# Optimization experiments

Hardware: AMD Instinct MI355X
Metric: run time of the kernel (lower is better)

## Reference

```python
import jax, jax.numpy as jnp
import numpy as np

B, N, D, H, DH, E, BIAS_DIM = 8, 512, 512, 8, 64, 32768, 8

def setup_inputs() -> dict:
    key = jax.random.key(0)
    ks = jax.random.split(key, 10)
    states = jax.random.normal(ks[0], (B, N, D), jnp.float32)
    key_states = jax.random.normal(ks[1], (B, N, D), jnp.float32)
    # causal mask, broadcastable over heads: [B,1,N,N]
    masks = jnp.broadcast_to(jnp.tril(jnp.ones((N, N), jnp.float32)), (B, 1, N, N))
    edge_type = jax.random.randint(ks[2], (E, 1), 0, BIAS_DIM, jnp.int32)
    b_idx = jax.random.randint(ks[3], (E, 1), 0, B, jnp.int32)
    q_idx = jax.random.randint(ks[4], (E, 1), 0, N, jnp.int32)
    k_idx = jax.random.randint(ks[5], (E, 1), 0, N, jnp.int32)
    attention_bias = jnp.concatenate([edge_type, b_idx, q_idx, k_idx], axis=1)
    s = 0.05
    Wq = jax.random.normal(ks[6], (D, H, DH), jnp.float32) * s
    Wk = jax.random.normal(ks[7], (D, H, DH), jnp.float32) * s
    Wv = jax.random.normal(ks[8], (D, H, DH), jnp.float32) * s
    k2 = jax.random.split(ks[9], 3)
    Wo = jax.random.normal(k2[0], (H, DH, D), jnp.float32) * s
    bias_embs = jax.random.normal(k2[1], (BIAS_DIM, DH), jnp.float32) * s
    bias_scalar = jax.random.normal(k2[2], (DH, 1), jnp.float32) * s
    return {"states": states, "key_states": key_states, "masks": masks,
            "attention_bias": attention_bias, "Wq": Wq, "Wk": Wk, "Wv": Wv,
            "Wo": Wo, "bias_embs": bias_embs, "bias_scalar": bias_scalar}

def reference(states, key_states, masks, attention_bias, Wq, Wk, Wv, Wo, bias_embs, bias_scalar):
    q = jnp.einsum('btd,dha->btha', states, Wq)
    k = jnp.einsum('btd,dha->btha', key_states, Wk)
    v = jnp.einsum('btd,dha->btha', key_states, Wv)
    alpha = jnp.einsum('bkha,bqha->bhqk', k, q)  # [B,H,Q,K]
    # sparse edge bias: embed edge types, project to scalar, scatter into [B,Q,K]
    et = attention_bias[:, 0]
    bias_vals = (bias_embs[et] @ bias_scalar)[:, 0]  # [E]
    bq, bk = alpha.shape[2], alpha.shape[3]
    bias_mat = jnp.zeros((alpha.shape[0], bq, bk), alpha.dtype)
    bias_mat = bias_mat.at[attention_bias[:, 1], attention_bias[:, 2], attention_bias[:, 3]].add(bias_vals)
    summed_keys = jnp.sum(k, axis=-1)  # [B,K,H]
    alpha = alpha + jnp.einsum('bqk,bkh->bhqk', bias_mat, summed_keys)
    alpha = alpha * jax.lax.rsqrt(jnp.float32(DH))
    neg = jnp.finfo(jnp.float32).min
    alpha = alpha * masks + (1.0 - jnp.ceil(masks)) * neg
    alpha = jax.nn.softmax(alpha, axis=-1)
    alpha = alpha * masks
    context = jnp.einsum('bhqk,bkha->bqha', alpha, v)
    return jnp.einsum('btha,had->btd', context, Wo)
```

## Files before the change

### kernel.cpp

```cpp
#include <hip/hip_runtime.h>

typedef unsigned short u16;
typedef unsigned int u32;
typedef __bf16 bf16x8 __attribute__((ext_vector_type(8)));
typedef float f32x4 __attribute__((ext_vector_type(4)));
typedef u16 u16x8 __attribute__((ext_vector_type(8)));
typedef u16 u16x4 __attribute__((ext_vector_type(4)));


__device__ __forceinline__ u16 f2b(float f) {
  union { float f; u32 i; } v; v.f = f;
  u32 r = v.i + 0x7fffu + ((v.i >> 16) & 1u);
  return (u16)(r >> 16);
}
__device__ __forceinline__ float b2f(u16 u) {
  union { u32 i; float f; } v; v.i = ((u32)u) << 16; return v.f;
}

#define GLL16(gp, lp)                                                      \
  __builtin_amdgcn_global_load_lds(                                       \
      (const __attribute__((address_space(1))) u32*)(gp),                 \
      (__attribute__((address_space(3))) u32*)(lp), 16, 0, 0)

__device__ __forceinline__ void stage64(const u16* g, u16* l, int wave, int lane) {
  int rsub = lane >> 3;
  int gs = (((lane & 7) ^ rsub) << 3);
  #pragma unroll
  for (int c = 0; c < 2; c++) {
    int ch = wave * 2 + c;
    GLL16(g + (size_t)(ch * 8 + rsub) * 512 + gs, l + ch * 512);
  }
}
__device__ __forceinline__ void stage128(const u16* g, u16* l, int wave, int lane) {
  int rsub = lane >> 3;
  int gs = (((lane & 7) ^ rsub) << 3);
  #pragma unroll
  for (int c = 0; c < 4; c++) {
    int ch = wave * 4 + c;
    GLL16(g + (size_t)(ch * 8 + rsub) * 512 + gs, l + ch * 512);
  }
}
__device__ __forceinline__ int swz(int row, int g) {
  return row * 64 + ((g ^ (row & 7)) << 3);
}

__global__ __launch_bounds__(256) void prologue(
    const float* __restrict__ states, const float* __restrict__ key_states,
    const float* __restrict__ Wq, const float* __restrict__ Wk,
    const float* __restrict__ Wv, const float* __restrict__ Wo,
    const int* __restrict__ ab, const float* __restrict__ be,
    const float* __restrict__ bsc,
    u16* __restrict__ sb, u16* __restrict__ kbin, u16* __restrict__ wbase,
    float* __restrict__ bias_mat, int n_edges) {
  __shared__ u16 t[32][33];
  __shared__ float tv[8];
  int bid = blockIdx.x;
  int tid = threadIdx.x;
  if (bid < 2048) {
    const float* src = (bid >= 1024) ? key_states : states;
    u16* dst = (bid >= 1024) ? kbin : sb;
    int gid = (bid & 1023) * 256 + tid;
    const float4* sp = (const float4*)src + (size_t)gid * 2;
    float4 x0 = sp[0], x1 = sp[1];
    u16x8 p;
    p[0] = f2b(x0.x); p[1] = f2b(x0.y); p[2] = f2b(x0.z); p[3] = f2b(x0.w);
    p[4] = f2b(x1.x); p[5] = f2b(x1.y); p[6] = f2b(x1.z); p[7] = f2b(x1.w);
    *(u16x8*)(dst + (size_t)gid * 8) = p;
  } else if (bid < 3072) {
    int tt = bid - 2048;
    int z = tt >> 8, rem = tt & 255;
    int bx = rem & 15, by = rem >> 4;
    const float* src; float sc = 1.f;
    if (z == 0)      { src = Wq; sc = 0.125f; }
    else if (z == 1) { src = Wk; }
    else if (z == 2) { src = Wv; }
    else             { src = Wo; }
    u16* dst = wbase + (size_t)z * 262144;
    int tx = tid & 31, ty = tid >> 5;
    int c0 = bx * 32, r0 = by * 32;
    #pragma unroll
    for (int i = ty; i < 32; i += 8) t[i][tx] = f2b(src[(r0 + i) * 512 + c0 + tx] * sc);
    __syncthreads();
    #pragma unroll
    for (int i = ty; i < 32; i += 8) dst[(c0 + i) * 512 + r0 + tx] = t[tx][i];
  } else {
    if (tid < 8) {
      float s = 0.f;
      #pragma unroll
      for (int a = 0; a < 64; a++) s += be[tid * 64 + a] * bsc[a];
      tv[tid] = s * 0.125f;
    }
    __syncthreads();
    int e = (bid - 3072) * 256 + tid;
    if (e < n_edges) {
      int et = ab[e * 4 + 0];
      int b  = ab[e * 4 + 1];
      int qi = ab[e * 4 + 2];
      int ki = ab[e * 4 + 3];
      atomicAdd(&bias_mat[((size_t)b * 512 + qi) * 512 + ki], tv[et]);
    }
  }
}

__global__ __launch_bounds__(256) void qkv_gemm(const u16* __restrict__ sb,
                                                const u16* __restrict__ kbin,
                                                const u16* __restrict__ wT,
                                                u16* __restrict__ qb,
                                                u16* __restrict__ kbo,
                                                u16* __restrict__ vtb,
                                                float* __restrict__ summed) {
  __shared__ alignas(16) u16 As[2][64 * 64];
  __shared__ alignas(16) u16 Bs[2][128 * 64];
  __shared__ float ssum[4][64];
  int tid = threadIdx.x;
  int lane = tid & 63, wave = tid >> 6;
  int quad = lane >> 4, ln = lane & 15;
  int row0 = blockIdx.x * 64;
  int col0 = blockIdx.y * 128;
  const u16* A = (col0 < 512) ? sb : kbin;
  const u16* Ab = A + (size_t)row0 * 512;
  const u16* Bb = wT + (size_t)col0 * 512;

  f32x4 acc[4][2];
  #pragma unroll
  for (int i = 0; i < 4; i++)
    #pragma unroll
    for (int j = 0; j < 2; j++) acc[i][j] = (f32x4){0.f, 0.f, 0.f, 0.f};

  stage64(Ab, As[0], wave, lane);
  stage128(Bb, Bs[0], wave, lane);

  int cur = 0;
  for (int k0 = 0; k0 < 512; k0 += 64) {
    __syncthreads();
    if (k0 < 448) {
      stage64(Ab + k0 + 64, As[cur ^ 1], wave, lane);
      stage128(Bb + k0 + 64, Bs[cur ^ 1], wave, lane);
    }
    #pragma unroll
    for (int s = 0; s < 2; s++) {
      bf16x8 af[4], bfv[2];
      #pragma unroll
      for (int i = 0; i < 4; i++)
        af[i] = *(bf16x8*)&As[cur][swz(i * 16 + ln, s * 4 + quad)];
      #pragma unroll
      for (int j = 0; j < 2; j++)
        bfv[j] = *(bf16x8*)&Bs[cur][swz(wave * 32 + j * 16 + ln, s * 4 + quad)];
      #pragma unroll
      for (int i = 0; i < 4; i++)
        #pragma unroll
        for (int j = 0; j < 2; j++)
          acc[i][j] = __builtin_amdgcn_mfma_f32_16x16x32_bf16(af[i], bfv[j], acc[i][j], 0, 0, 0);
    }
    cur ^= 1;
  }

  int region = col0 >> 9;
  int nbase = col0 & 511;
  if (region <= 1) {
    u16* Cout = region ? kbo : qb;
    #pragma unroll
    for (int i = 0; i < 4; i++)
      #pragma unroll
      for (int j = 0; j < 2; j++) {
        int mb = row0 + i * 16 + quad * 4;
        int n = nbase + wave * 32 + j * 16 + ln;
        #pragma unroll
        for (int r = 0; r < 4; r++)
          Cout[(size_t)(mb + r) * 512 + n] = f2b(acc[i][j][r]);
      }
    if (region == 1) {
      #pragma unroll
      for (int i = 0; i < 4; i++)
        #pragma unroll
        for (int r = 0; r < 4; r++) {
          float v = acc[i][0][r] + acc[i][1][r];
          v += __shfl_xor(v, 1);
          v += __shfl_xor(v, 2);
          v += __shfl_xor(v, 4);
          v += __shfl_xor(v, 8);
          if (ln == 0) ssum[wave][i * 16 + quad * 4 + r] = v;
        }
      __syncthreads();
      if (tid < 128) {
        int hl = tid >> 6, row = tid & 63;
        float s = ssum[hl * 2][row] + ssum[hl * 2 + 1][row];
        int m = row0 + row;
        int b = m >> 9, t = m & 511;
        int h = (nbase >> 6) + hl;
        summed[((size_t)(b * 8 + h)) * 512 + t] = s;
      }
    }
  } else {
    #pragma unroll
    for (int i = 0; i < 4; i++)
      #pragma unroll
      for (int j = 0; j < 2; j++) {
        int mb = row0 + i * 16 + quad * 4;
        int bb = mb >> 9, t0 = mb & 511;
        int a_abs = nbase + wave * 32 + j * 16 + ln;
        int h = a_abs >> 6, a = a_abs & 63;
        u16x4 p;
        p[0] = f2b(acc[i][j][0]); p[1] = f2b(acc[i][j][1]);
        p[2] = f2b(acc[i][j][2]); p[3] = f2b(acc[i][j][3]);
        *(u16x4*)&vtb[(((size_t)bb * 8 + h) * 64 + a) * 512 + t0] = p;
      }
  }
}

__global__ __launch_bounds__(256) void out_gemm(const u16* __restrict__ A,
                                                const u16* __restrict__ BT,
                                                float* __restrict__ C) {
  __shared__ alignas(16) u16 As[2][64 * 64];
  __shared__ alignas(16) u16 Bs[2][64 * 64];
  int tid = threadIdx.x;
  int lane = tid & 63, wave = tid >> 6;
  int quad = lane >> 4, ln = lane & 15;
  int wr = wave >> 1, wc = wave & 1;
  int row0 = blockIdx.x * 64;
  int col0 = blockIdx.y * 64;
  const u16* Ab = A + (size_t)row0 * 512;
  const u16* Bb = BT + (size_t)col0 * 512;

  f32x4 acc[2][2];
  #pragma unroll
  for (int i = 0; i < 2; i++)
    #pragma unroll
    for (int j = 0; j < 2; j++) acc[i][j] = (f32x4){0.f, 0.f, 0.f, 0.f};

  stage64(Ab, As[0], wave, lane);
  stage64(Bb, Bs[0], wave, lane);

  int cur = 0;
  for (int k0 = 0; k0 < 512; k0 += 64) {
    __syncthreads();
    if (k0 < 448) {
      stage64(Ab + k0 + 64, As[cur ^ 1], wave, lane);
      stage64(Bb + k0 + 64, Bs[cur ^ 1], wave, lane);
    }
    #pragma unroll
    for (int s = 0; s < 2; s++) {
      bf16x8 af[2], bfv[2];
      #pragma unroll
      for (int i = 0; i < 2; i++)
        af[i] = *(bf16x8*)&As[cur][swz(wr * 32 + i * 16 + ln, s * 4 + quad)];
      #pragma unroll
      for (int j = 0; j < 2; j++)
        bfv[j] = *(bf16x8*)&Bs[cur][swz(wc * 32 + j * 16 + ln, s * 4 + quad)];
      #pragma unroll
      for (int i = 0; i < 2; i++)
        #pragma unroll
        for (int j = 0; j < 2; j++)
          acc[i][j] = __builtin_amdgcn_mfma_f32_16x16x32_bf16(af[i], bfv[j], acc[i][j], 0, 0, 0);
    }
    cur ^= 1;
  }
  #pragma unroll
  for (int i = 0; i < 2; i++)
    #pragma unroll
    for (int j = 0; j < 2; j++) {
      int mb = row0 + wr * 32 + i * 16 + quad * 4;
      int n = col0 + wc * 32 + j * 16 + ln;
      #pragma unroll
      for (int r = 0; r < 4; r++)
        C[(size_t)(mb + r) * 512 + n] = acc[i][j][r];
    }
}

__global__ __launch_bounds__(256) void attn_mfma(const u16* __restrict__ q,
                                                 const u16* __restrict__ k,
                                                 const u16* __restrict__ vt,
                                                 const float* __restrict__ bias_mat,
                                                 const float* __restrict__ summed,
                                                 u16* __restrict__ ctx,
                                                 float* __restrict__ Opart,
                                                 float* __restrict__ ml) {
  __shared__ alignas(16) u16 Qs[64 * 64];
  __shared__ alignas(16) u16 Ks[2][64 * 64];
  __shared__ alignas(16) u16 Vs[2][64 * 64];
  __shared__ alignas(16) u16 Ps[4][16 * 72];
  int tid = threadIdx.x;
  int wave = tid >> 6, lane = tid & 63;
  int quad = lane >> 4, ln = lane & 15;
  int p2 = blockIdx.x;
  int bh, u;
  {
    const int fours[6] = {3, 4, 6, 8, 10, 11};
    const int threes[2] = {2, 9};
    const int ones[2] = {0, 5};
    const int twos[2] = {1, 7};
    if (p2 < 384)      { bh = p2 & 63; u = fours[p2 >> 6]; }
    else if (p2 < 512) { int q2 = p2 - 384; bh = q2 & 63; u = threes[q2 >> 6]; }
    else if (p2 < 640) { int q2 = p2 - 512; bh = q2 & 63; u = ones[q2 >> 6]; }
    else               { int q2 = p2 - 640; bh = q2 & 63; u = twos[q2 >> 6]; }
  }
  int b = bh >> 3, h = bh & 7;
  int qt, kb0, kbe, part = 0;
  bool partial;
  if (u < 4) { qt = u; kb0 = 0; kbe = u; partial = false; }
  else {
    int v = u - 4; qt = 4 + (v >> 1); part = v & 1; partial = true;
    if (part == 0) { kb0 = 0; kbe = 3; } else { kb0 = 4; kbe = qt; }
  }
  int q0 = qt * 64;

  const u16* qb_ = q + ((size_t)(b * 512 + q0)) * 512 + h * 64;
  const u16* kb_ = k + ((size_t)(b * 512)) * 512 + h * 64;
  const u16* vb_ = vt + ((size_t)bh * 64) * 512;

  stage64(qb_, Qs, wave, lane);
  stage64(kb_ + (size_t)kb0 * 64 * 512, Ks[0], wave, lane);
  stage64(vb_ + kb0 * 64, Vs[0], wave, lane);

  float m_r[4], l_r[4];
  f32x4 o[4];
  #pragma unroll
  for (int r = 0; r < 4; r++) { m_r[r] = -3.40282347e38f; l_r[r] = 0.f; }
  #pragma unroll
  for (int nt = 0; nt < 4; nt++) o[nt] = (f32x4){0.f, 0.f, 0.f, 0.f};

  int qrow = q0 + wave * 16 + quad * 4;

  float c_skv[4], c_bias[4][4];
  #pragma unroll
  for (int nt = 0; nt < 4; nt++) {
    int t = kb0 * 64 + nt * 16 + ln;
    c_skv[nt] = summed[bh * 512 + t];
    const float* bp2 = bias_mat + ((size_t)(b * 512 + qrow)) * 512 + t;
    #pragma unroll
    for (int r = 0; r < 4; r++) c_bias[nt][r] = bp2[(size_t)r * 512];
  }

  int cur = 0;
  for (int kb = kb0; kb <= kbe; kb++) {
    __syncthreads();

    float n_skv[4], n_bias[4][4];
    if (kb < kbe) {
      stage64(kb_ + (size_t)(kb + 1) * 64 * 512, Ks[cur ^ 1], wave, lane);
      stage64(vb_ + (kb + 1) * 64, Vs[cur ^ 1], wave, lane);
      #pragma unroll
      for (int nt = 0; nt < 4; nt++) {
        int t = (kb + 1) * 64 + nt * 16 + ln;
        n_skv[nt] = summed[bh * 512 + t];
        const float* bp2 = bias_mat + ((size_t)(b * 512 + qrow)) * 512 + t;
        #pragma unroll
        for (int r = 0; r < 4; r++) n_bias[nt][r] = bp2[(size_t)r * 512];
      }
    }

    bf16x8 aq0 = *(bf16x8*)&Qs[swz(wave * 16 + ln, quad)];
    bf16x8 aq1 = *(bf16x8*)&Qs[swz(wave * 16 + ln, 4 + quad)];
    f32x4 s[4];
    #pragma unroll
    for (int nt = 0; nt < 4; nt++) {
      bf16x8 b0 = *(bf16x8*)&Ks[cur][swz(nt * 16 + ln, quad)];
      bf16x8 b1 = *(bf16x8*)&Ks[cur][swz(nt * 16 + ln, 4 + quad)];
      s[nt] = (f32x4){0.f, 0.f, 0.f, 0.f};
      s[nt] = __builtin_amdgcn_mfma_f32_16x16x32_bf16(aq0, b0, s[nt], 0, 0, 0);
      s[nt] = __builtin_amdgcn_mfma_f32_16x16x32_bf16(aq1, b1, s[nt], 0, 0, 0);
    }

    #pragma unroll
    for (int nt = 0; nt < 4; nt++) {
      int t = kb * 64 + nt * 16 + ln;
      #pragma unroll
      for (int r = 0; r < 4; r++) {
        float val = s[nt][r] + c_bias[nt][r] * c_skv[nt];
        s[nt][r] = (t <= qrow + r) ? val : -3.40282347e38f;
      }
    }

    float alpha[4];
    #pragma unroll
    for (int r = 0; r < 4; r++) {
      float tm = fmaxf(fmaxf(s[0][r], s[1][r]), fmaxf(s[2][r], s[3][r]));
      #pragma unroll
      for (int off = 8; off; off >>= 1) tm = fmaxf(tm, __shfl_xor(tm, off));
      float mn = fmaxf(m_r[r], tm);
      alpha[r] = __expf(m_r[r] - mn);
      m_r[r] = mn;
      float rs = 0.f;
      #pragma unroll
      for (int nt = 0; nt < 4; nt++) {
        float pp = __expf(s[nt][r] - mn);
        s[nt][r] = pp;
        rs += pp;
      }
      #pragma unroll
      for (int off = 8; off; off >>= 1) rs += __shfl_xor(rs, off);
      l_r[r] = l_r[r] * alpha[r] + rs;
    }

    #pragma unroll
    for (int nt = 0; nt < 4; nt++)
      #pragma unroll
      for (int r = 0; r < 4; r++)
        Ps[wave][(quad * 4 + r) * 72 + nt * 16 + ln] = f2b(s[nt][r]);
    #pragma unroll
    for (int nt = 0; nt < 4; nt++)
      #pragma unroll
      for (int r = 0; r < 4; r++)
        o[nt][r] *= alpha[r];

    bf16x8 ap0 = *(bf16x8*)&Ps[wave][ln * 72 + quad * 8];
    bf16x8 ap1 = *(bf16x8*)&Ps[wave][ln * 72 + 32 + quad * 8];
    #pragma unroll
    for (int nt = 0; nt < 4; nt++) {
      bf16x8 b0 = *(bf16x8*)&Vs[cur][swz(nt * 16 + ln, quad)];
      bf16x8 b1 = *(bf16x8*)&Vs[cur][swz(nt * 16 + ln, 4 + quad)];
      o[nt] = __builtin_amdgcn_mfma_f32_16x16x32_bf16(ap0, b0, o[nt], 0, 0, 0);
      o[nt] = __builtin_amdgcn_mfma_f32_16x16x32_bf16(ap1, b1, o[nt], 0, 0, 0);
    }

    if (kb < kbe) {
      #pragma unroll
      for (int nt = 0; nt < 4; nt++) {
        c_skv[nt] = n_skv[nt];
        #pragma unroll
        for (int r = 0; r < 4; r++) c_bias[nt][r] = n_bias[nt][r];
      }
    }
    cur ^= 1;
  }

  if (!partial) {
    #pragma unroll
    for (int r = 0; r < 4; r++) {
      float inv = 1.f / l_r[r];
      int qr2 = qrow + r;
      u16* dst = ctx + ((size_t)(b * 512 + qr2)) * 512 + h * 64;
      #pragma unroll
      for (int nt = 0; nt < 4; nt++)
        dst[nt * 16 + ln] = f2b(o[nt][r] * inv);
    }
  } else {
    #pragma unroll
    for (int r = 0; r < 4; r++) {
      int row = qrow + r - 256;
      float* dst = Opart + (((size_t)(part * 64 + bh)) * 256 + row) * 64;
      #pragma unroll
      for (int nt = 0; nt < 4; nt++)
        dst[nt * 16 + ln] = o[nt][r];
    }
    if (ln == 0) {
      #pragma unroll
      for (int r = 0; r < 4; r++) {
        int row = qrow + r - 256;
        float* mp = ml + (((size_t)(part * 64 + bh)) * 256 + row) * 2;
        mp[0] = m_r[r];
        mp[1] = l_r[r];
      }
    }
  }
}

__global__ __launch_bounds__(256) void attn_merge(const float* __restrict__ Opart,
                                                  const float* __restrict__ ml,
                                                  u16* __restrict__ ctx) {
  int gid = blockIdx.x * 256 + threadIdx.x;
  int col = gid & 63;
  int row = (gid >> 6) & 255;
  int bh = gid >> 14;
  size_t i0 = (size_t)bh * 256 + row;
  size_t i1 = (size_t)(64 + bh) * 256 + row;
  float m0 = ml[i0 * 2], l0 = ml[i0 * 2 + 1];
  float m1 = ml[i1 * 2], l1 = ml[i1 * 2 + 1];
  float m = fmaxf(m0, m1);
  float a0 = __expf(m0 - m), a1 = __expf(m1 - m);
  float l = l0 * a0 + l1 * a1;
  float O0 = Opart[i0 * 64 + col], O1 = Opart[i1 * 64 + col];
  float val = (O0 * a0 + O1 * a1) / l;
  int b = bh >> 3, h = bh & 7, qrow = 256 + row;
  ctx[((size_t)(b * 512 + qrow)) * 512 + h * 64 + col] = f2b(val);
}

extern "C" void kernel_launch(void* const* d_in, const int* in_sizes, int n_in,
                              void* d_out, int out_size, void* d_ws, size_t ws_size,
                              hipStream_t stream) {
  const float* states     = (const float*)d_in[0];
  const float* key_states = (const float*)d_in[1];
  const int*   ab         = (const int*)d_in[3];
  const float* Wq         = (const float*)d_in[4];
  const float* Wk         = (const float*)d_in[5];
  const float* Wv         = (const float*)d_in[6];
  const float* Wo         = (const float*)d_in[7];
  const float* be         = (const float*)d_in[8];
  const float* bsc        = (const float*)d_in[9];
  float* out = (float*)d_out;

  char* ws = (char*)d_ws;
  const size_t MB = 1024 * 1024;
  u16* wbase    = (u16*)(ws);
  u16* wot      = (u16*)(ws + 1536 * 1024);
  u16* sb       = (u16*)(ws + 2 * MB);
  u16* kbin     = (u16*)(ws + 6 * MB);
  u16* qb       = (u16*)(ws + 10 * MB);
  u16* kbo      = (u16*)(ws + 14 * MB);
  u16* vtb      = (u16*)(ws + 18 * MB);
  u16* ctxb     = (u16*)(ws + 22 * MB);
  float* bias_m = (float*)(ws + 26 * MB);
  float* summed = (float*)(ws + 34 * MB);
  float* Opart  = (float*)(ws + 35 * MB);
  float* mlbuf  = (float*)(ws + 43 * MB);

  int n_edges = in_sizes[3] / 4;

  hipMemsetAsync(bias_m, 0, (size_t)8 * MB, stream);
  prologue<<<dim3(3072 + (n_edges + 255) / 256), 256, 0, stream>>>(
      states, key_states, Wq, Wk, Wv, Wo, ab, be, bsc, sb, kbin, wbase, bias_m, n_edges);
  qkv_gemm<<<dim3(64, 12), 256, 0, stream>>>(sb, kbin, wbase, qb, kbo, vtb, summed);
  attn_mfma<<<dim3(768), 256, 0, stream>>>(qb, kbo, vtb, bias_m, summed, ctxb, Opart, mlbuf);
  attn_merge<<<dim3(4096), 256, 0, stream>>>(Opart, mlbuf, ctxb);
  out_gemm<<<dim3(64, 8), 256, 0, stream>>>(ctxb, wot, out);
}
```

Before: 134.6 us.

## Fuse bias zeroing, edge scatter and split-softmax merge into neighbouring kernels

Removes the hipMemset and has prologue zero the bias matrix with float4 stores. Moves the edge bias scatter (atomicAdd) into qkv_gemm blocks. Drops the separate attn_merge kernel and merges the split-KV partials inside out_gemm's A-tile staging for rows 256-511. Together these cut two launches and a round trip of ctx through global memory. In exchange, merged tiles use register loads plus LDS stores instead of async global_load_lds, and the atomic scatter delays the start of the GEMM.

```diff
diff --git a/kernel.cpp b/kernel.cpp
--- a/kernel.cpp
+++ b/kernel.cpp
@@ -13,9 +13,6 @@
   u32 r = v.i + 0x7fffu + ((v.i >> 16) & 1u);
   return (u16)(r >> 16);
 }
-__device__ __forceinline__ float b2f(u16 u) {
-  union { u32 i; float f; } v; v.i = ((u32)u) << 16; return v.f;
-}
 
 #define GLL16(gp, lp)                                                      \
   __builtin_amdgcn_global_load_lds(                                       \
@@ -48,12 +45,9 @@
     const float* __restrict__ states, const float* __restrict__ key_states,
     const float* __restrict__ Wq, const float* __restrict__ Wk,
     const float* __restrict__ Wv, const float* __restrict__ Wo,
-    const int* __restrict__ ab, const float* __restrict__ be,
-    const float* __restrict__ bsc,
     u16* __restrict__ sb, u16* __restrict__ kbin, u16* __restrict__ wbase,
-    float* __restrict__ bias_mat, int n_edges) {
+    float* __restrict__ bias_mat) {
   __shared__ u16 t[32][33];
-  __shared__ float tv[8];
   int bid = blockIdx.x;
   int tid = threadIdx.x;
   if (bid < 2048) {
@@ -84,37 +78,53 @@
     #pragma unroll
     for (int i = ty; i < 32; i += 8) dst[(c0 + i) * 512 + r0 + tx] = t[tx][i];
   } else {
-    if (tid < 8) {
-      float s = 0.f;
-      #pragma unroll
-      for (int a = 0; a < 64; a++) s += be[tid * 64 + a] * bsc[a];
-      tv[tid] = s * 0.125f;
-    }
-    __syncthreads();
-    int e = (bid - 3072) * 256 + tid;
-    if (e < n_edges) {
-      int et = ab[e * 4 + 0];
-      int b  = ab[e * 4 + 1];
-      int qi = ab[e * 4 + 2];
-      int ki = ab[e * 4 + 3];
-      atomicAdd(&bias_mat[((size_t)b * 512 + qi) * 512 + ki], tv[et]);
-    }
+    int i = (bid - 3072) * 256 + tid;
+    float4 z4 = {0.f, 0.f, 0.f, 0.f};
+    ((float4*)bias_mat)[i] = z4;
   }
 }
 
 __global__ __launch_bounds__(256) void qkv_gemm(const u16* __restrict__ sb,
                                                 const u16* __restrict__ kbin,
                                                 const u16* __restrict__ wT,
+                                                const int* __restrict__ ab,
+                                                const float* __restrict__ be,
+                                                const float* __restrict__ bsc,
+                                                float* __restrict__ bias_m,
                                                 u16* __restrict__ qb,
                                                 u16* __restrict__ kbo,
                                                 u16* __restrict__ vtb,
-                                                float* __restrict__ summed) {
+                                                float* __restrict__ summed,
+                                                int n_edges) {
   __shared__ alignas(16) u16 As[2][64 * 64];
   __shared__ alignas(16) u16 Bs[2][128 * 64];
   __shared__ float ssum[4][64];
+  __shared__ float tvs[8];
   int tid = threadIdx.x;
   int lane = tid & 63, wave = tid >> 6;
   int quad = lane >> 4, ln = lane & 15;
+  int fb = blockIdx.y * 64 + blockIdx.x;
+
+  if (tid < 8) {
+    const float4* bev = (const float4*)(be + tid * 64);
+    const float4* bscv = (const float4*)bsc;
+    float s = 0.f;
+    #pragma unroll
+    for (int a4 = 0; a4 < 16; a4++) {
+      float4 x = bev[a4], y = bscv[a4];
+      s += x.x * y.x + x.y * y.y + x.z * y.z + x.w * y.w;
+    }
+    tvs[tid] = s * 0.125f;
+  }
+  __syncthreads();
+  for (int e = fb * 256 + tid; e < n_edges; e += 768 * 256) {
+    int et = ab[e * 4 + 0];
+    int b  = ab[e * 4 + 1];
+    int qi = ab[e * 4 + 2];
+    int ki = ab[e * 4 + 3];
+    atomicAdd(&bias_m[((size_t)b * 512 + qi) * 512 + ki], tvs[et]);
+  }
+
   int row0 = blockIdx.x * 64;
   int col0 = blockIdx.y * 128;
   const u16* A = (col0 < 512) ? sb : kbin;
@@ -206,65 +216,6 @@
         *(u16x4*)&vtb[(((size_t)bb * 8 + h) * 64 + a) * 512 + t0] = p;
       }
   }
-}
-
-__global__ __launch_bounds__(256) void out_gemm(const u16* __restrict__ A,
-                                                const u16* __restrict__ BT,
-                                                float* __restrict__ C) {
-  __shared__ alignas(16) u16 As[2][64 * 64];
-  __shared__ alignas(16) u16 Bs[2][64 * 64];
-  int tid = threadIdx.x;
-  int lane = tid & 63, wave = tid >> 6;
-  int quad = lane >> 4, ln = lane & 15;
-  int wr = wave >> 1, wc = wave & 1;
-  int row0 = blockIdx.x * 64;
-  int col0 = blockIdx.y * 64;
-  const u16* Ab = A + (size_t)row0 * 512;
-  const u16* Bb = BT + (size_t)col0 * 512;
-
-  f32x4 acc[2][2];
-  #pragma unroll
-  for (int i = 0; i < 2; i++)
-    #pragma unroll
-    for (int j = 0; j < 2; j++) acc[i][j] = (f32x4){0.f, 0.f, 0.f, 0.f};
-
-  stage64(Ab, As[0], wave, lane);
-  stage64(Bb, Bs[0], wave, lane);
-
-  int cur = 0;
-  for (int k0 = 0; k0 < 512; k0 += 64) {
-    __syncthreads();
-    if (k0 < 448) {
-      stage64(Ab + k0 + 64, As[cur ^ 1], wave, lane);
-      stage64(Bb + k0 + 64, Bs[cur ^ 1], wave, lane);
-    }
-    #pragma unroll
-    for (int s = 0; s < 2; s++) {
-      bf16x8 af[2], bfv[2];
-      #pragma unroll
-      for (int i = 0; i < 2; i++)
-        af[i] = *(bf16x8*)&As[cur][swz(wr * 32 + i * 16 + ln, s * 4 + quad)];
-      #pragma unroll
-      for (int j = 0; j < 2; j++)
-        bfv[j] = *(bf16x8*)&Bs[cur][swz(wc * 32 + j * 16 + ln, s * 4 + quad)];
-      #pragma unroll
-      for (int i = 0; i < 2; i++)
-        #pragma unroll
-        for (int j = 0; j < 2; j++)
-          acc[i][j] = __builtin_amdgcn_mfma_f32_16x16x32_bf16(af[i], bfv[j], acc[i][j], 0, 0, 0);
-    }
-    cur ^= 1;
-  }
-  #pragma unroll
-  for (int i = 0; i < 2; i++)
-    #pragma unroll
-    for (int j = 0; j < 2; j++) {
-      int mb = row0 + wr * 32 + i * 16 + quad * 4;
-      int n = col0 + wc * 32 + j * 16 + ln;
-      #pragma unroll
-      for (int r = 0; r < 4; r++)
-        C[(size_t)(mb + r) * 512 + n] = acc[i][j][r];
-    }
 }
 
 __global__ __launch_bounds__(256) void attn_mfma(const u16* __restrict__ q,
@@ -455,24 +406,107 @@
   }
 }
 
-__global__ __launch_bounds__(256) void attn_merge(const float* __restrict__ Opart,
-                                                  const float* __restrict__ ml,
-                                                  u16* __restrict__ ctx) {
-  int gid = blockIdx.x * 256 + threadIdx.x;
-  int col = gid & 63;
-  int row = (gid >> 6) & 255;
-  int bh = gid >> 14;
-  size_t i0 = (size_t)bh * 256 + row;
-  size_t i1 = (size_t)(64 + bh) * 256 + row;
-  float m0 = ml[i0 * 2], l0 = ml[i0 * 2 + 1];
-  float m1 = ml[i1 * 2], l1 = ml[i1 * 2 + 1];
+__device__ __forceinline__ void merge_stage(const float* __restrict__ Opart,
+                                            const float* __restrict__ mlbuf,
+                                            int row0, int k0, u16* dst, int tid) {
+  int gi = tid * 2;
+  int r = gi >> 3, g = gi & 7;
+  int trow = (row0 & 511) - 256 + r;
+  int b = row0 >> 9;
+  int h = k0 >> 6;
+  size_t i0 = ((size_t)(b * 8 + h)) * 256 + trow;
+  size_t i1 = i0 + 64 * 256;
+  float m0 = mlbuf[i0 * 2], l0 = mlbuf[i0 * 2 + 1];
+  float m1 = mlbuf[i1 * 2], l1 = mlbuf[i1 * 2 + 1];
   float m = fmaxf(m0, m1);
   float a0 = __expf(m0 - m), a1 = __expf(m1 - m);
-  float l = l0 * a0 + l1 * a1;
-  float O0 = Opart[i0 * 64 + col], O1 = Opart[i1 * 64 + col];
-  float val = (O0 * a0 + O1 * a1) / l;
-  int b = bh >> 3, h = bh & 7, qrow = 256 + row;
-  ctx[((size_t)(b * 512 + qrow)) * 512 + h * 64 + col] = f2b(val);
+  float linv = 1.f / (l0 * a0 + l1 * a1);
+  a0 *= linv; a1 *= linv;
+  const float4* p0 = (const float4*)(Opart + i0 * 64 + g * 8);
+  const float4* p1 = (const float4*)(Opart + i1 * 64 + g * 8);
+  u16x8 q0, q1;
+  #pragma unroll
+  for (int c = 0; c < 2; c++) {
+    float4 x0 = p0[c], x1 = p1[c];
+    q0[c * 4 + 0] = f2b(x0.x * a0 + x1.x * a1);
+    q0[c * 4 + 1] = f2b(x0.y * a0 + x1.y * a1);
+    q0[c * 4 + 2] = f2b(x0.z * a0 + x1.z * a1);
+    q0[c * 4 + 3] = f2b(x0.w * a0 + x1.w * a1);
+  }
+  #pragma unroll
+  for (int c = 2; c < 4; c++) {
+    float4 x0 = p0[c], x1 = p1[c];
+    q1[(c - 2) * 4 + 0] = f2b(x0.x * a0 + x1.x * a1);
+    q1[(c - 2) * 4 + 1] = f2b(x0.y * a0 + x1.y * a1);
+    q1[(c - 2) * 4 + 2] = f2b(x0.z * a0 + x1.z * a1);
+    q1[(c - 2) * 4 + 3] = f2b(x0.w * a0 + x1.w * a1);
+  }
+  *(u16x8*)&dst[swz(r, g)] = q0;
+  *(u16x8*)&dst[swz(r, g + 1)] = q1;
+}
+
+__global__ __launch_bounds__(256) void out_gemm(const u16* __restrict__ A,
+                                                const u16* __restrict__ BT,
+                                                const float* __restrict__ Opart,
+                                                const float* __restrict__ mlbuf,
+                                                float* __restrict__ C) {
+  __shared__ alignas(16) u16 As[2][64 * 64];
+  __shared__ alignas(16) u16 Bs[2][64 * 64];
+  int tid = threadIdx.x;
+  int lane = tid & 63, wave = tid >> 6;
+  int quad = lane >> 4, ln = lane & 15;
+  int wr = wave >> 1, wc = wave & 1;
+  int row0 = blockIdx.x * 64;
+  int col0 = blockIdx.y * 64;
+  bool mergeA = (row0 & 511) >= 256;
+  const u16* Ab = A + (size_t)row0 * 512;
+  const u16* Bb = BT + (size_t)col0 * 512;
+
+  f32x4 acc[2][2];
+  #pragma unroll
+  for (int i = 0; i < 2; i++)
+    #pragma unroll
+    for (int j = 0; j < 2; j++) acc[i][j] = (f32x4){0.f, 0.f, 0.f, 0.f};
+
+  if (mergeA) merge_stage(Opart, mlbuf, row0, 0, As[0], tid);
+  else        stage64(Ab, As[0], wave, lane);
+  stage64(Bb, Bs[0], wave, lane);
+
+  int cur = 0;
+  for (int k0 = 0; k0 < 512; k0 += 64) {
+    __syncthreads();
+    if (k0 < 448) {
+      if (mergeA) merge_stage(Opart, mlbuf, row0, k0 + 64, As[cur ^ 1], tid);
+      else        stage64(Ab + k0 + 64, As[cur ^ 1], wave, lane);
+      stage64(Bb + k0 + 64, Bs[cur ^ 1], wave, lane);
+    }
+    #pragma unroll
+    for (int s = 0; s < 2; s++) {
+      bf16x8 af[2], bfv[2];
+      #pragma unroll
+      for (int i = 0; i < 2; i++)
+        af[i] = *(bf16x8*)&As[cur][swz(wr * 32 + i * 16 + ln, s * 4 + quad)];
+      #pragma unroll
+      for (int j = 0; j < 2; j++)
+        bfv[j] = *(bf16x8*)&Bs[cur][swz(wc * 32 + j * 16 + ln, s * 4 + quad)];
+      #pragma unroll
+      for (int i = 0; i < 2; i++)
+        #pragma unroll
+        for (int j = 0; j < 2; j++)
+          acc[i][j] = __builtin_amdgcn_mfma_f32_16x16x32_bf16(af[i], bfv[j], acc[i][j], 0, 0, 0);
+    }
+    cur ^= 1;
+  }
+  #pragma unroll
+  for (int i = 0; i < 2; i++)
+    #pragma unroll
+    for (int j = 0; j < 2; j++) {
+      int mb = row0 + wr * 32 + i * 16 + quad * 4;
+      int n = col0 + wc * 32 + j * 16 + ln;
+      #pragma unroll
+      for (int r = 0; r < 4; r++)
+        C[(size_t)(mb + r) * 512 + n] = acc[i][j][r];
+    }
 }
 
 extern "C" void kernel_launch(void* const* d_in, const int* in_sizes, int n_in,
@@ -506,11 +540,10 @@
 
   int n_edges = in_sizes[3] / 4;
 
-  hipMemsetAsync(bias_m, 0, (size_t)8 * MB, stream);
-  prologue<<<dim3(3072 + (n_edges + 255) / 256), 256, 0, stream>>>(
-      states, key_states, Wq, Wk, Wv, Wo, ab, be, bsc, sb, kbin, wbase, bias_m, n_edges);
-  qkv_gemm<<<dim3(64, 12), 256, 0, stream>>>(sb, kbin, wbase, qb, kbo, vtb, summed);
+  prologue<<<dim3(5120), 256, 0, stream>>>(
+      states, key_states, Wq, Wk, Wv, Wo, sb, kbin, wbase, bias_m);
+  qkv_gemm<<<dim3(64, 12), 256, 0, stream>>>(
+      sb, kbin, wbase, ab, be, bsc, bias_m, qb, kbo, vtb, summed, n_edges);
   attn_mfma<<<dim3(768), 256, 0, stream>>>(qb, kbo, vtb, bias_m, summed, ctxb, Opart, mlbuf);
-  attn_merge<<<dim3(4096), 256, 0, stream>>>(Opart, mlbuf, ctxb);
-  out_gemm<<<dim3(64, 8), 256, 0, stream>>>(ctxb, wot, out);
-}
+  out_gemm<<<dim3(64, 8), 256, 0, stream>>>(ctxb, wot, Opart, mlbuf, out);
+}
```

After: 133.5 us. Within noise of the previous version (-0.8%).
